# Optimization experiments

Hardware: AMD Instinct MI355X
Metric: run time of the kernel (lower is better)

The kernel has to match this reference:

```python
import jax, jax.numpy as jnp
import numpy as np

BS, SEQ, VOCAB, EMS, NHID, ML = 32, 512, 5000, 256, 512, 16
TEMP = 0.9
GAMMA = 0.0  # self.gamma is a fixed zero Variable in the original


def setup_inputs() -> dict:
    key = jax.random.key(0)
    ks = jax.random.split(key, 10)
    nm = SEQ // ML
    inputs = jax.random.randint(ks[0], (BS, SEQ), 0, VOCAB, dtype=jnp.int32)
    measure_steps = jax.random.randint(ks[1], (ML, BS, nm), 0, VOCAB, dtype=jnp.int32)
    measure_weights = jax.random.normal(ks[2], (BS, nm, nm), dtype=jnp.float32)
    h0 = jnp.zeros((BS, NHID), jnp.float32)
    c0 = jnp.zeros((BS, NHID), jnp.float32)
    initrange = 0.1
    emb = jax.random.uniform(ks[3], (VOCAB, EMS), minval=-initrange, maxval=initrange)
    k = 1.0 / np.sqrt(NHID).astype(np.float32)
    W_ih = jax.random.uniform(ks[4], (4 * NHID, EMS), minval=-k, maxval=k)
    W_hh = jax.random.uniform(ks[5], (4 * NHID, NHID), minval=-k, maxval=k)
    b_ih = jax.random.uniform(ks[6], (4 * NHID,), minval=-k, maxval=k)
    b_hh = jax.random.uniform(ks[7], (4 * NHID,), minval=-k, maxval=k)
    W_dec = jax.random.uniform(ks[8], (VOCAB, NHID), minval=-initrange, maxval=initrange)
    b_dec = jnp.zeros((VOCAB,), jnp.float32)
    return dict(inputs=inputs, h0=h0, c0=c0, measure_weights=measure_weights,
                measure_steps=measure_steps, emb=emb, W_ih=W_ih, W_hh=W_hh,
                b_ih=b_ih, b_hh=b_hh, W_dec=W_dec, b_dec=b_dec, measure_length=ML)


def _forward(h0, c0, mw, emb, W_ih, W_hh, b_ih, b_hh, W_dec, b_dec,
             inputs, msteps, measure_length):
    bs, seq = inputs.shape
    nm = seq // measure_length
    # attention over previous measures: softmax over j < m (causal-masked)
    mask = (jnp.arange(nm)[None, :] < jnp.arange(nm)[:, None]).astype(mw.dtype)  # [m, j]
    logits = jnp.where(mask[None] > 0, mw / TEMP, -1e9)
    sm = jax.nn.softmax(logits, axis=-1) * mask[None]  # [bs, m, j]
    prev_embs = emb[msteps]  # [ML, bs, nm, E]
    # lookback embedding for (measure m, step s): sum_j sm[b,m,j] * emb[steps[s,b,j]]
    lb = jnp.einsum('bmj,sbje->msbe', sm, prev_embs)  # [nm, ML, bs, E]
    lb_seq = lb.reshape(seq, bs, -1)  # time-major: t = m*ML + s
    # per-step bmm decode against embedding table: [bs, seq, V]
    lookback = jnp.einsum('tbe,ve->btv', lb_seq, emb)
    # original zeros lookback for timesteps with int(i/num_measures)==0, i.e. i < nm
    tmask = (jnp.arange(seq) >= nm)[None, :, None]
    lookback = jnp.where(tmask, lookback, jnp.zeros((), lookback.dtype))

    x = emb[inputs]  # [bs, seq, E] (single channel -> concat is identity)

    def cell(carry, xt):
        h, c = carry
        g = xt @ W_ih.T + b_ih + h @ W_hh.T + b_hh
        i, f, gg, o = jnp.split(g, 4, axis=-1)
        c2 = jax.nn.sigmoid(f) * c + jax.nn.sigmoid(i) * jnp.tanh(gg)
        h2 = jax.nn.sigmoid(o) * jnp.tanh(c2)
        return (h2, c2), h2

    (hT, cT), hs = jax.lax.scan(cell, (h0, c0), jnp.swapaxes(x, 0, 1))
    out = jnp.swapaxes(hs, 0, 1)  # [bs, seq, nhid]
    decoded = out @ W_dec.T + b_dec  # [bs, seq, V]
    dec = (1.0 - GAMMA) * decoded + GAMMA * lookback
    return dec, hT, cT


def reference(inputs, h0, c0, measure_weights, measure_steps, emb,
              W_ih, W_hh, b_ih, b_hh, W_dec, b_dec, measure_length):
    return _forward(h0, c0, measure_weights, emb, W_ih, W_hh, b_ih, b_hh,
                    W_dec, b_dec, inputs, measure_steps, measure_length)
```

## Files before the change

### kernel.cpp

```cpp
#include <hip/hip_runtime.h>
#include <cstdint>
#include <cstddef>

#define BS     32
#define SEQ    512
#define VOCAB  5000
#define EMS    256
#define NHID   512
#define GH     2048
#define NWG    32
#define SLICE  16
#define VPAD   5120
#define NBLK   256
#define NDEC   (NBLK - NWG)
#define NTILE  ((BS*SEQ/128) * (VPAD/128))

#define WS_FLAGS 0
#define WS_BIAS  2048
#define WS_WIH   (WS_BIAS + GH*4)
#define WS_WHH   (WS_WIH + GH*EMS*2)
#define WS_WDH   (WS_WHH + GH*NHID*2)
#define WS_WDL   (WS_WDH + VPAD*NHID*2)
#define WS_X     (WS_WDL + VPAD*NHID*2)
#define WS_HHI   (WS_X + SEQ*BS*EMS*2)
#define WS_HLO   (WS_HHI + BS*SEQ*NHID*2)
#define WS_HBUF  (WS_HLO + BS*SEQ*NHID*2)
#define WS_END   (WS_HBUF + 2*BS*NHID*2)

typedef float f32x4 __attribute__((ext_vector_type(4)));
typedef __bf16 bf16x8 __attribute__((ext_vector_type(8)));

static __device__ __forceinline__ uint16_t f2bf(float x) {
  uint32_t u = __builtin_bit_cast(uint32_t, x);
  u += 0x7FFFu + ((u >> 16) & 1u);
  return (uint16_t)(u >> 16);
}
static __device__ __forceinline__ float bf2f(uint16_t b) {
  return __builtin_bit_cast(float, (uint32_t)b << 16);
}
static __device__ __forceinline__ float sigf(float x) { return 1.0f / (1.0f + __expf(-x)); }
static __device__ __forceinline__ float tanhf_fast(float x) {
  return 1.0f - 2.0f / (__expf(2.0f * x) + 1.0f);
}
static __device__ __forceinline__ f32x4 mfma16(uint4 a, uint4 b, f32x4 c) {
  return __builtin_amdgcn_mfma_f32_16x16x32_bf16(
      __builtin_bit_cast(bf16x8, a), __builtin_bit_cast(bf16x8, b), c, 0, 0, 0);
}
static __device__ __forceinline__ void glds16(const void* g, void* l) {
  __builtin_amdgcn_global_load_lds((__attribute__((address_space(1))) void*)g,
                                   (__attribute__((address_space(3))) void*)l,
                                   16, 0, 0);
}
static __device__ __forceinline__ void coh_store_u32(uint32_t* p, uint32_t v) {
  __hip_atomic_store(p, v, __ATOMIC_RELAXED, __HIP_MEMORY_SCOPE_AGENT);
}

__global__ __launch_bounds__(256) void prep_kernel(
    const int* __restrict__ inputs, const float* __restrict__ h0,
    const float* __restrict__ emb, const float* __restrict__ Wih,
    const float* __restrict__ Whh, const float* __restrict__ bih,
    const float* __restrict__ bhh, const float* __restrict__ Wd,
    char* __restrict__ ws) {
  int gid = blockIdx.x * 256 + threadIdx.x;
  int gsz = gridDim.x * 256;
  uint16_t* wX  = (uint16_t*)(ws + WS_X);
  uint16_t* wIH = (uint16_t*)(ws + WS_WIH);
  uint16_t* wHH = (uint16_t*)(ws + WS_WHH);
  uint16_t* wDH = (uint16_t*)(ws + WS_WDH);
  uint16_t* wDL = (uint16_t*)(ws + WS_WDL);
  float*    bias = (float*)(ws + WS_BIAS);
  uint16_t* hb  = (uint16_t*)(ws + WS_HBUF);
  if (gid < 512) ((uint32_t*)(ws + WS_FLAGS))[gid] = 0u;
  for (int i = gid; i < SEQ*BS*EMS; i += gsz) {
    int e = i & (EMS-1), b = (i >> 8) & (BS-1), t = i >> 13;
    wX[i] = f2bf(emb[(size_t)inputs[b*SEQ + t] * EMS + e]);
  }
  for (int i = gid; i < GH*EMS; i += gsz)  wIH[i] = f2bf(Wih[i]);
  for (int i = gid; i < GH*NHID; i += gsz) wHH[i] = f2bf(Whh[i]);
  for (int i = gid; i < VPAD*NHID; i += gsz) {
    int row = i >> 9;
    uint16_t hi = 0, lo = 0;
    if (row < VOCAB) {
      float x = Wd[i];
      hi = f2bf(x);
      lo = f2bf(x - bf2f(hi));
    }
    wDH[i] = hi; wDL[i] = lo;
  }
  for (int i = gid; i < GH; i += gsz) bias[i] = bih[i] + bhh[i];
  for (int i = gid; i < BS*NHID; i += gsz) hb[i] = f2bf(h0[i]);
}

__global__ __launch_bounds__(256, 1) void fused_kernel(
    char* __restrict__ ws, const float* __restrict__ c0,
    const float* __restrict__ bdec, float* __restrict__ out,
    float* __restrict__ outT) {
  __shared__ __align__(16) char smem[104 * 1024];
  uint32_t* flags = (uint32_t*)(ws + WS_FLAGS);
  const int tid = threadIdx.x;
  const int lane = tid & 63, w = tid >> 6;

  if (blockIdx.x < NWG) {
    char* sW = smem;
    char* sH = smem + 64*1024;
    float* sG = (float*)(smem + 96*1024);
    const uint16_t* wHH = (const uint16_t*)(ws + WS_WHH);
    const uint16_t* wIH = (const uint16_t*)(ws + WS_WIH);
    const uint16_t* wX  = (const uint16_t*)(ws + WS_X);
    const float* bias = (const float*)(ws + WS_BIAS);
    uint16_t* hbuf = (uint16_t*)(ws + WS_HBUF);
    uint16_t* Hhi  = (uint16_t*)(ws + WS_HHI);
    uint16_t* Hlo  = (uint16_t*)(ws + WS_HLO);
    const int wg = blockIdx.x;
    const int mw = w >> 1, nw = w & 1;

    for (int c = tid; c < 4096; c += 256) {
      int row = c >> 6;
      int kb = (c & 63) * 16;
      int G = row >> 4, dl = row & 15;
      uint4 v = *(const uint4*)(wHH + (size_t)(G*NHID + wg*SLICE + dl) * NHID + kb/2);
      *(uint4*)(sW + row*1024 + (kb ^ ((row & 7) << 4))) = v;
    }
    const int bq = tid >> 3, dq = (tid & 7) * 2;
    float c_0 = c0[bq*NHID + wg*SLICE + dq];
    float c_1 = c0[bq*NHID + wg*SLICE + dq + 1];
    const int arow = mw*16 + (lane & 15);
    const int brow0 = (2*nw)*16 + (lane & 15);
    const int brow1 = brow0 + 16;
    const int kb0 = (lane >> 4) * 16;
    const int kfrag = (lane >> 4) * 8;
    const float bs0 = bias[(2*nw+0)*NHID + wg*SLICE + (lane & 15)];
    const float bs1 = bias[(2*nw+1)*NHID + wg*SLICE + (lane & 15)];
    uint4 wbf[2][8];
#pragma unroll
    for (int g = 0; g < 2; ++g)
#pragma unroll
      for (int k2 = 0; k2 < 8; ++k2)
        wbf[g][k2] = *(const uint4*)(wIH +
            (size_t)((2*nw+g)*NHID + wg*SLICE + (lane & 15)) * EMS + k2*32 + kfrag);
    uint4 xa[8], xb[8];
#pragma unroll
    for (int k2 = 0; k2 < 8; ++k2)
      xa[k2] = *(const uint4*)(wX + (size_t)arow * EMS + k2*32 + kfrag);
    __syncthreads();

    for (int t = 0; t < SEQ; ++t) {
      if (t > 0) {
        const uint32_t tgt = (uint32_t)t;
        const uint32_t* fp = flags + (lane & 31) * 16;
        uint32_t ptries = 0;
        for (;;) {
          uint32_t v = __hip_atomic_load(fp, __ATOMIC_RELAXED, __HIP_MEMORY_SCOPE_AGENT);
          if (__all((int)(v >= tgt))) break;
          if (++ptries > (1u << 20)) break;
        }
      }

      uint4 v0, v1, v2, v3, v4, v5, v6, v7;
      {
        const char* pb = (const char*)(hbuf + (t & 1) * (BS*NHID)) + tid * 16;
        asm volatile("global_load_dwordx4 %0, %1, off sc0 sc1" : "=v"(v0) : "v"(pb));
        asm volatile("global_load_dwordx4 %0, %1, off sc0 sc1" : "=v"(v1) : "v"(pb + 4096));
        asm volatile("global_load_dwordx4 %0, %1, off sc0 sc1" : "=v"(v2) : "v"(pb + 8192));
        asm volatile("global_load_dwordx4 %0, %1, off sc0 sc1" : "=v"(v3) : "v"(pb + 12288));
        asm volatile("global_load_dwordx4 %0, %1, off sc0 sc1" : "=v"(v4) : "v"(pb + 16384));
        asm volatile("global_load_dwordx4 %0, %1, off sc0 sc1" : "=v"(v5) : "v"(pb + 20480));
        asm volatile("global_load_dwordx4 %0, %1, off sc0 sc1" : "=v"(v6) : "v"(pb + 24576));
        asm volatile("global_load_dwordx4 %0, %1, off sc0 sc1" : "=v"(v7) : "v"(pb + 28672));
        const int tn = (t + 1 < SEQ) ? (t + 1) : 0;
        const uint16_t* xp = wX + (size_t)(tn*BS + arow) * EMS + kfrag;
        asm volatile("global_load_dwordx4 %0, %1, off"             : "=v"(xb[0]) : "v"(xp));
        asm volatile("global_load_dwordx4 %0, %1, off offset:64"   : "=v"(xb[1]) : "v"(xp));
        asm volatile("global_load_dwordx4 %0, %1, off offset:128"  : "=v"(xb[2]) : "v"(xp));
        asm volatile("global_load_dwordx4 %0, %1, off offset:192"  : "=v"(xb[3]) : "v"(xp));
        asm volatile("global_load_dwordx4 %0, %1, off offset:256"  : "=v"(xb[4]) : "v"(xp));
        asm volatile("global_load_dwordx4 %0, %1, off offset:320"  : "=v"(xb[5]) : "v"(xp));
        asm volatile("global_load_dwordx4 %0, %1, off offset:384"  : "=v"(xb[6]) : "v"(xp));
        asm volatile("global_load_dwordx4 %0, %1, off offset:448"  : "=v"(xb[7]) : "v"(xp));
      }
      f32x4 acc0, acc1;
#pragma unroll
      for (int r = 0; r < 4; ++r) { acc0[r] = bs0; acc1[r] = bs1; }
#pragma unroll
      for (int k2 = 0; k2 < 8; ++k2) {
        acc0 = mfma16(xa[k2], wbf[0][k2], acc0);
        acc1 = mfma16(xa[k2], wbf[1][k2], acc1);
      }
      asm volatile("s_waitcnt vmcnt(8)" ::: "memory");
      __builtin_amdgcn_sched_barrier(0);
      {
        const int kb = (tid & 63) * 16;
        const int ww = tid >> 6;
#define STW(J, VJ) *(uint4*)(sH + ((J)*4 + ww)*1024 + (kb ^ ((((J)&1)*4 + ww) << 4))) = VJ;
        STW(0, v0) STW(1, v1) STW(2, v2) STW(3, v3)
        STW(4, v4) STW(5, v5) STW(6, v6) STW(7, v7)
#undef STW
      }
      __syncthreads();

#pragma unroll
      for (int kt = 0; kt < 16; ++kt) {
        int kb = kt*64 + kb0;
        uint4 av = *(const uint4*)(sH + arow*1024 + (kb ^ ((arow & 7) << 4)));
        uint4 b0 = *(const uint4*)(sW + brow0*1024 + (kb ^ ((brow0 & 7) << 4)));
        uint4 b1 = *(const uint4*)(sW + brow1*1024 + (kb ^ ((brow1 & 7) << 4)));
        acc0 = mfma16(av, b0, acc0);
        acc1 = mfma16(av, b1, acc1);
      }
#pragma unroll
      for (int r = 0; r < 4; ++r) {
        int b = mw*16 + (lane >> 4)*4 + r;
        sG[((2*nw+0)*BS + b)*SLICE + (lane & 15)] = acc0[r];
        sG[((2*nw+1)*BS + b)*SLICE + (lane & 15)] = acc1[r];
      }
#pragma unroll
      for (int k2 = 0; k2 < 8; ++k2) xa[k2] = xb[k2];
      __syncthreads();

      float gi0 = sG[(0*BS + bq)*SLICE + dq], gi1 = sG[(0*BS + bq)*SLICE + dq + 1];
      float gf0 = sG[(1*BS + bq)*SLICE + dq], gf1 = sG[(1*BS + bq)*SLICE + dq + 1];
      float gg0 = sG[(2*BS + bq)*SLICE + dq], gg1 = sG[(2*BS + bq)*SLICE + dq + 1];
      float go0 = sG[(3*BS + bq)*SLICE + dq], go1 = sG[(3*BS + bq)*SLICE + dq + 1];
      c_0 = sigf(gf0)*c_0 + sigf(gi0)*tanhf_fast(gg0);
      c_1 = sigf(gf1)*c_1 + sigf(gi1)*tanhf_fast(gg1);
      float h_0 = sigf(go0)*tanhf_fast(c_0);
      float h_1 = sigf(go1)*tanhf_fast(c_1);

      uint16_t hh0 = f2bf(h_0), hh1 = f2bf(h_1);
      uint32_t hp = (uint32_t)hh0 | ((uint32_t)hh1 << 16);
      coh_store_u32((uint32_t*)(hbuf + ((t+1) & 1)*(BS*NHID)) +
                        ((bq*NHID + wg*SLICE + dq) >> 1), hp);
      size_t hoff = ((size_t)t*BS + bq)*NHID + wg*SLICE + dq;
      coh_store_u32((uint32_t*)(Hhi + hoff), hp);
      uint32_t lp = (uint32_t)f2bf(h_0 - bf2f(hh0)) | ((uint32_t)f2bf(h_1 - bf2f(hh1)) << 16);
      coh_store_u32((uint32_t*)(Hlo + hoff), lp);
      if (t == SEQ-1) {
        outT[bq*NHID + wg*SLICE + dq]     = h_0;
        outT[bq*NHID + wg*SLICE + dq + 1] = h_1;
        outT[BS*NHID + bq*NHID + wg*SLICE + dq]     = c_0;
        outT[BS*NHID + bq*NHID + wg*SLICE + dq + 1] = c_1;
      }

      __syncthreads();
      if (tid == 0)
        __hip_atomic_store(flags + wg * 16, (uint32_t)(t + 1),
                           __ATOMIC_RELAXED, __HIP_MEMORY_SCOPE_AGENT);
    }
  } else {
    char* lds = smem;
    const uint16_t* Hhi = (const uint16_t*)(ws + WS_HHI);
    const uint16_t* Hlo = (const uint16_t*)(ws + WS_HLO);
    const uint16_t* WDH = (const uint16_t*)(ws + WS_WDH);
    const uint16_t* WDL = (const uint16_t*)(ws + WS_WDL);
    const int widx = (int)blockIdx.x - NWG;
    const int wbase = (tid & ~63);
    const int mq = (w >> 1) * 64, nq = (w & 1) * 64;

    for (int q = widx; q < NTILE; q += NDEC) {
      const int mt = q / 40, nt = q % 40;
      const int m0 = mt * 128, n0 = nt * 128;
      if (w == 0) {
        const uint32_t tgt = (uint32_t)(mt*4 + 4);
        const uint32_t* fp = flags + (lane & 31) * 16;
        uint32_t tries = 0;
        for (;;) {
          uint32_t v = __hip_atomic_load(fp, __ATOMIC_RELAXED, __HIP_MEMORY_SCOPE_AGENT);
          if (__all((int)(v >= tgt))) break;
          __builtin_amdgcn_s_sleep(64);
          if (++tries > (1u << 14)) break;
        }
      }
      __syncthreads();

      auto stage = [&](int buf, int kk) {
        char* base = lds + buf * 32768;
#pragma unroll
        for (int c2 = 0; c2 < 2; ++c2) {
          int idx = c2*256 + tid;
          int row = idx >> 2, col = (idx & 3) * 8;
          int ldst = (c2*256 + wbase) * 16;
          glds16(Hhi + (size_t)(m0 + row) * NHID + kk*32 + col, base + ldst);
          glds16(Hlo + (size_t)(m0 + row) * NHID + kk*32 + col, base + 8192 + ldst);
          glds16(WDH + (size_t)(n0 + row) * NHID + kk*32 + col, base + 16384 + ldst);
          glds16(WDL + (size_t)(n0 + row) * NHID + kk*32 + col, base + 24576 + ldst);
        }
      };

      const f32x4 zero = {0.f, 0.f, 0.f, 0.f};
      f32x4 acc[4][4];
#pragma unroll
      for (int i = 0; i < 4; ++i)
#pragma unroll
        for (int j = 0; j < 4; ++j) acc[i][j] = zero;

      stage(0, 0);
      for (int s = 0; s < 16; ++s) {
        __syncthreads();
        if (s + 1 < 16) stage((s + 1) & 1, s + 1);
        const char* cb = lds + (s & 1) * 32768;
        uint4 ahi[4], alo[4], bhi[4], blo[4];
#pragma unroll
        for (int i = 0; i < 4; ++i) {
          int aoff = (mq + i*16 + (lane & 15))*64 + (lane >> 4)*16;
          int boff = (nq + i*16 + (lane & 15))*64 + (lane >> 4)*16;
          ahi[i] = *(const uint4*)(cb + aoff);
          alo[i] = *(const uint4*)(cb + 8192 + aoff);
          bhi[i] = *(const uint4*)(cb + 16384 + boff);
          blo[i] = *(const uint4*)(cb + 24576 + boff);
        }
#pragma unroll
        for (int i = 0; i < 4; ++i)
#pragma unroll
          for (int j = 0; j < 4; ++j) {
            acc[i][j] = mfma16(ahi[i], bhi[j], acc[i][j]);
            acc[i][j] = mfma16(ahi[i], blo[j], acc[i][j]);
            acc[i][j] = mfma16(alo[i], bhi[j], acc[i][j]);
          }
      }
#pragma unroll
      for (int j = 0; j < 4; ++j) {
        int V = n0 + nq + j*16 + (lane & 15);
        if (V >= VOCAB) continue;
        float bv = bdec[V];
#pragma unroll
        for (int i = 0; i < 4; ++i) {
          int Rb = m0 + mq + i*16 + (lane >> 4)*4;
#pragma unroll
          for (int r = 0; r < 4; ++r) {
            int rr = Rb + r;
            int orow = (rr & 31) * SEQ + (rr >> 5);
            out[(size_t)orow * VOCAB + V] = acc[i][j][r] + bv;
          }
        }
      }
      __syncthreads();
    }
  }
}

extern "C" void kernel_launch(void* const* d_in, const int* in_sizes, int n_in,
                              void* d_out, int out_size, void* d_ws, size_t ws_size,
                              hipStream_t stream) {
  (void)in_sizes; (void)n_in; (void)out_size; (void)ws_size;
  const int*   inputs = (const int*)  d_in[0];
  const float* h0     = (const float*)d_in[1];
  const float* c0     = (const float*)d_in[2];
  const float* emb    = (const float*)d_in[5];
  const float* Wih    = (const float*)d_in[6];
  const float* Whh    = (const float*)d_in[7];
  const float* bih    = (const float*)d_in[8];
  const float* bhh    = (const float*)d_in[9];
  const float* Wdec   = (const float*)d_in[10];
  const float* bdec   = (const float*)d_in[11];
  char* ws   = (char*)d_ws;
  float* out = (float*)d_out;
  float* outT = out + (size_t)BS*SEQ*VOCAB;

  prep_kernel<<<512, 256, 0, stream>>>(inputs, h0, emb, Wih, Whh, bih, bhh, Wdec, ws);
  fused_kernel<<<NBLK, 256, 0, stream>>>(ws, c0, bdec, out, outT);
}
```

Measured before the change: 2.085 ms.

## Split fused persistent kernel into separate LSTM scan and decoder GEMM kernels

Replaces the single persistent kernel, where 32 blocks ran the LSTM recurrence while the other blocks polled flags and decoded tiles as they became ready, with two launches: a 32-block scan kernel and a full-grid decode GEMM kernel. Hidden states are now stored batch-major with plain stores instead of coherent stores. This lets the decoder write output rows contiguously and use a swizzled tile order. The decode kernel now uses all CUs without flag waits, but decoding no longer overlaps with the serial recurrence, so the decoder GEMM time is added after the scan.

```diff
diff --git a/kernel.cpp b/kernel.cpp
--- a/kernel.cpp
+++ b/kernel.cpp
@@ -11,8 +11,6 @@
 #define NWG    32
 #define SLICE  16
 #define VPAD   5120
-#define NBLK   256
-#define NDEC   (NBLK - NWG)
 #define NTILE  ((BS*SEQ/128) * (VPAD/128))
 
 #define WS_FLAGS 0
@@ -91,249 +89,231 @@
   for (int i = gid; i < BS*NHID; i += gsz) hb[i] = f2bf(h0[i]);
 }
 
-__global__ __launch_bounds__(256, 1) void fused_kernel(
-    char* __restrict__ ws, const float* __restrict__ c0,
-    const float* __restrict__ bdec, float* __restrict__ out,
-    float* __restrict__ outT) {
-  __shared__ __align__(16) char smem[104 * 1024];
+__global__ __launch_bounds__(256, 1) void scan_kernel(
+    char* __restrict__ ws, const float* __restrict__ c0, float* __restrict__ outT) {
+  __shared__ __align__(16) char sW[64*1024];
+  __shared__ __align__(16) char sH[32*1024];
+  __shared__ float sG[4*BS*SLICE];
   uint32_t* flags = (uint32_t*)(ws + WS_FLAGS);
+  const uint16_t* wHH = (const uint16_t*)(ws + WS_WHH);
+  const uint16_t* wIH = (const uint16_t*)(ws + WS_WIH);
+  const uint16_t* wX  = (const uint16_t*)(ws + WS_X);
+  const float* bias = (const float*)(ws + WS_BIAS);
+  uint16_t* hbuf = (uint16_t*)(ws + WS_HBUF);
+  uint16_t* Hhi  = (uint16_t*)(ws + WS_HHI);
+  uint16_t* Hlo  = (uint16_t*)(ws + WS_HLO);
+  const int tid = threadIdx.x, wg = blockIdx.x;
+  const int lane = tid & 63, w = tid >> 6;
+  const int mw = w >> 1, nw = w & 1;
+
+  for (int c = tid; c < 4096; c += 256) {
+    int row = c >> 6;
+    int kb = (c & 63) * 16;
+    int G = row >> 4, dl = row & 15;
+    uint4 v = *(const uint4*)(wHH + (size_t)(G*NHID + wg*SLICE + dl) * NHID + kb/2);
+    *(uint4*)(sW + row*1024 + (kb ^ ((row & 7) << 4))) = v;
+  }
+  const int bq = tid >> 3, dq = (tid & 7) * 2;
+  float c_0 = c0[bq*NHID + wg*SLICE + dq];
+  float c_1 = c0[bq*NHID + wg*SLICE + dq + 1];
+  const int arow = mw*16 + (lane & 15);
+  const int brow0 = (2*nw)*16 + (lane & 15);
+  const int brow1 = brow0 + 16;
+  const int kb0 = (lane >> 4) * 16;
+  const int kfrag = (lane >> 4) * 8;
+  const float bs0 = bias[(2*nw+0)*NHID + wg*SLICE + (lane & 15)];
+  const float bs1 = bias[(2*nw+1)*NHID + wg*SLICE + (lane & 15)];
+  uint4 wbf[2][8];
+#pragma unroll
+  for (int g = 0; g < 2; ++g)
+#pragma unroll
+    for (int k2 = 0; k2 < 8; ++k2)
+      wbf[g][k2] = *(const uint4*)(wIH +
+          (size_t)((2*nw+g)*NHID + wg*SLICE + (lane & 15)) * EMS + k2*32 + kfrag);
+  uint4 xa[8], xb[8];
+#pragma unroll
+  for (int k2 = 0; k2 < 8; ++k2)
+    xa[k2] = *(const uint4*)(wX + (size_t)arow * EMS + k2*32 + kfrag);
+  __syncthreads();
+
+  for (int t = 0; t < SEQ; ++t) {
+    if (t > 0) {
+      const uint32_t tgt = (uint32_t)t;
+      const uint32_t* fp = flags + (lane & 31) * 16;
+      uint32_t ptries = 0;
+      for (;;) {
+        uint32_t v = __hip_atomic_load(fp, __ATOMIC_RELAXED, __HIP_MEMORY_SCOPE_AGENT);
+        if (__all((int)(v >= tgt))) break;
+        if (++ptries > (1u << 20)) break;
+      }
+    }
+
+    uint4 v0, v1, v2, v3, v4, v5, v6, v7;
+    {
+      const char* pb = (const char*)(hbuf + (t & 1) * (BS*NHID)) + tid * 16;
+      asm volatile("global_load_dwordx4 %0, %1, off sc0 sc1" : "=v"(v0) : "v"(pb));
+      asm volatile("global_load_dwordx4 %0, %1, off sc0 sc1" : "=v"(v1) : "v"(pb + 4096));
+      asm volatile("global_load_dwordx4 %0, %1, off sc0 sc1" : "=v"(v2) : "v"(pb + 8192));
+      asm volatile("global_load_dwordx4 %0, %1, off sc0 sc1" : "=v"(v3) : "v"(pb + 12288));
+      asm volatile("global_load_dwordx4 %0, %1, off sc0 sc1" : "=v"(v4) : "v"(pb + 16384));
+      asm volatile("global_load_dwordx4 %0, %1, off sc0 sc1" : "=v"(v5) : "v"(pb + 20480));
+      asm volatile("global_load_dwordx4 %0, %1, off sc0 sc1" : "=v"(v6) : "v"(pb + 24576));
+      asm volatile("global_load_dwordx4 %0, %1, off sc0 sc1" : "=v"(v7) : "v"(pb + 28672));
+      const int tn = (t + 1 < SEQ) ? (t + 1) : 0;
+      const uint16_t* xp = wX + (size_t)(tn*BS + arow) * EMS + kfrag;
+      asm volatile("global_load_dwordx4 %0, %1, off"             : "=v"(xb[0]) : "v"(xp));
+      asm volatile("global_load_dwordx4 %0, %1, off offset:64"   : "=v"(xb[1]) : "v"(xp));
+      asm volatile("global_load_dwordx4 %0, %1, off offset:128"  : "=v"(xb[2]) : "v"(xp));
+      asm volatile("global_load_dwordx4 %0, %1, off offset:192"  : "=v"(xb[3]) : "v"(xp));
+      asm volatile("global_load_dwordx4 %0, %1, off offset:256"  : "=v"(xb[4]) : "v"(xp));
+      asm volatile("global_load_dwordx4 %0, %1, off offset:320"  : "=v"(xb[5]) : "v"(xp));
+      asm volatile("global_load_dwordx4 %0, %1, off offset:384"  : "=v"(xb[6]) : "v"(xp));
+      asm volatile("global_load_dwordx4 %0, %1, off offset:448"  : "=v"(xb[7]) : "v"(xp));
+    }
+    f32x4 acc0, acc1;
+#pragma unroll
+    for (int r = 0; r < 4; ++r) { acc0[r] = bs0; acc1[r] = bs1; }
+#pragma unroll
+    for (int k2 = 0; k2 < 8; ++k2) {
+      acc0 = mfma16(xa[k2], wbf[0][k2], acc0);
+      acc1 = mfma16(xa[k2], wbf[1][k2], acc1);
+    }
+    asm volatile("s_waitcnt vmcnt(8)" ::: "memory");
+    __builtin_amdgcn_sched_barrier(0);
+    {
+      const int kb = (tid & 63) * 16;
+      const int ww = tid >> 6;
+#define STW(J, VJ) *(uint4*)(sH + ((J)*4 + ww)*1024 + (kb ^ ((((J)&1)*4 + ww) << 4))) = VJ;
+      STW(0, v0) STW(1, v1) STW(2, v2) STW(3, v3)
+      STW(4, v4) STW(5, v5) STW(6, v6) STW(7, v7)
+#undef STW
+    }
+    __syncthreads();
+
+#pragma unroll
+    for (int kt = 0; kt < 16; ++kt) {
+      int kb = kt*64 + kb0;
+      uint4 av = *(const uint4*)(sH + arow*1024 + (kb ^ ((arow & 7) << 4)));
+      uint4 b0 = *(const uint4*)(sW + brow0*1024 + (kb ^ ((brow0 & 7) << 4)));
+      uint4 b1 = *(const uint4*)(sW + brow1*1024 + (kb ^ ((brow1 & 7) << 4)));
+      acc0 = mfma16(av, b0, acc0);
+      acc1 = mfma16(av, b1, acc1);
+    }
+#pragma unroll
+    for (int r = 0; r < 4; ++r) {
+      int b = mw*16 + (lane >> 4)*4 + r;
+      sG[((2*nw+0)*BS + b)*SLICE + (lane & 15)] = acc0[r];
+      sG[((2*nw+1)*BS + b)*SLICE + (lane & 15)] = acc1[r];
+    }
+    asm volatile("s_waitcnt vmcnt(0)" ::: "memory");
+#pragma unroll
+    for (int k2 = 0; k2 < 8; ++k2) xa[k2] = xb[k2];
+    __syncthreads();
+
+    float gi0 = sG[(0*BS + bq)*SLICE + dq], gi1 = sG[(0*BS + bq)*SLICE + dq + 1];
+    float gf0 = sG[(1*BS + bq)*SLICE + dq], gf1 = sG[(1*BS + bq)*SLICE + dq + 1];
+    float gg0 = sG[(2*BS + bq)*SLICE + dq], gg1 = sG[(2*BS + bq)*SLICE + dq + 1];
+    float go0 = sG[(3*BS + bq)*SLICE + dq], go1 = sG[(3*BS + bq)*SLICE + dq + 1];
+    c_0 = sigf(gf0)*c_0 + sigf(gi0)*tanhf_fast(gg0);
+    c_1 = sigf(gf1)*c_1 + sigf(gi1)*tanhf_fast(gg1);
+    float h_0 = sigf(go0)*tanhf_fast(c_0);
+    float h_1 = sigf(go1)*tanhf_fast(c_1);
+
+    uint16_t hh0 = f2bf(h_0), hh1 = f2bf(h_1);
+    uint32_t hp = (uint32_t)hh0 | ((uint32_t)hh1 << 16);
+    coh_store_u32((uint32_t*)(hbuf + ((t+1) & 1)*(BS*NHID)) +
+                      ((bq*NHID + wg*SLICE + dq) >> 1), hp);
+    size_t hoff = ((size_t)bq*SEQ + t)*NHID + wg*SLICE + dq;
+    *(uint32_t*)(Hhi + hoff) = hp;
+    uint32_t lp = (uint32_t)f2bf(h_0 - bf2f(hh0)) | ((uint32_t)f2bf(h_1 - bf2f(hh1)) << 16);
+    *(uint32_t*)(Hlo + hoff) = lp;
+    if (t == SEQ-1) {
+      outT[bq*NHID + wg*SLICE + dq]     = h_0;
+      outT[bq*NHID + wg*SLICE + dq + 1] = h_1;
+      outT[BS*NHID + bq*NHID + wg*SLICE + dq]     = c_0;
+      outT[BS*NHID + bq*NHID + wg*SLICE + dq + 1] = c_1;
+    }
+
+    __syncthreads();
+    if (tid == 0)
+      __hip_atomic_store(flags + wg * 16, (uint32_t)(t + 1),
+                         __ATOMIC_RELAXED, __HIP_MEMORY_SCOPE_AGENT);
+  }
+}
+
+__global__ __launch_bounds__(256) void decode_kernel(
+    const char* __restrict__ ws, const float* __restrict__ bdec,
+    float* __restrict__ out) {
+  __shared__ __align__(16) char lds[2][32768];
+  const uint16_t* Hhi = (const uint16_t*)(ws + WS_HHI);
+  const uint16_t* Hlo = (const uint16_t*)(ws + WS_HLO);
+  const uint16_t* WDH = (const uint16_t*)(ws + WS_WDH);
+  const uint16_t* WDL = (const uint16_t*)(ws + WS_WDL);
   const int tid = threadIdx.x;
   const int lane = tid & 63, w = tid >> 6;
-
-  if (blockIdx.x < NWG) {
-    char* sW = smem;
-    char* sH = smem + 64*1024;
-    float* sG = (float*)(smem + 96*1024);
-    const uint16_t* wHH = (const uint16_t*)(ws + WS_WHH);
-    const uint16_t* wIH = (const uint16_t*)(ws + WS_WIH);
-    const uint16_t* wX  = (const uint16_t*)(ws + WS_X);
-    const float* bias = (const float*)(ws + WS_BIAS);
-    uint16_t* hbuf = (uint16_t*)(ws + WS_HBUF);
-    uint16_t* Hhi  = (uint16_t*)(ws + WS_HHI);
-    uint16_t* Hlo  = (uint16_t*)(ws + WS_HLO);
-    const int wg = blockIdx.x;
-    const int mw = w >> 1, nw = w & 1;
-
-    for (int c = tid; c < 4096; c += 256) {
-      int row = c >> 6;
-      int kb = (c & 63) * 16;
-      int G = row >> 4, dl = row & 15;
-      uint4 v = *(const uint4*)(wHH + (size_t)(G*NHID + wg*SLICE + dl) * NHID + kb/2);
-      *(uint4*)(sW + row*1024 + (kb ^ ((row & 7) << 4))) = v;
-    }
-    const int bq = tid >> 3, dq = (tid & 7) * 2;
-    float c_0 = c0[bq*NHID + wg*SLICE + dq];
-    float c_1 = c0[bq*NHID + wg*SLICE + dq + 1];
-    const int arow = mw*16 + (lane & 15);
-    const int brow0 = (2*nw)*16 + (lane & 15);
-    const int brow1 = brow0 + 16;
-    const int kb0 = (lane >> 4) * 16;
-    const int kfrag = (lane >> 4) * 8;
-    const float bs0 = bias[(2*nw+0)*NHID + wg*SLICE + (lane & 15)];
-    const float bs1 = bias[(2*nw+1)*NHID + wg*SLICE + (lane & 15)];
-    uint4 wbf[2][8];
-#pragma unroll
-    for (int g = 0; g < 2; ++g)
-#pragma unroll
-      for (int k2 = 0; k2 < 8; ++k2)
-        wbf[g][k2] = *(const uint4*)(wIH +
-            (size_t)((2*nw+g)*NHID + wg*SLICE + (lane & 15)) * EMS + k2*32 + kfrag);
-    uint4 xa[8], xb[8];
-#pragma unroll
-    for (int k2 = 0; k2 < 8; ++k2)
-      xa[k2] = *(const uint4*)(wX + (size_t)arow * EMS + k2*32 + kfrag);
+  const int wbase = (tid & ~63);
+  const int mq = (w >> 1) * 64, nq = (w & 1) * 64;
+  const int bid = (int)blockIdx.x;
+  const int swz = (bid & 7) * (NTILE / 8) + (bid >> 3);
+  const int mt = swz / 40, nt = swz % 40;
+  const int m0 = mt * 128, n0 = nt * 128;
+
+  auto stage = [&](int buf, int kk) {
+    char* base = &lds[buf][0];
+#pragma unroll
+    for (int c2 = 0; c2 < 2; ++c2) {
+      int idx = c2*256 + tid;
+      int row = idx >> 2, col = (idx & 3) * 8;
+      int ldst = (c2*256 + wbase) * 16;
+      glds16(Hhi + (size_t)(m0 + row) * NHID + kk*32 + col, base + ldst);
+      glds16(Hlo + (size_t)(m0 + row) * NHID + kk*32 + col, base + 8192 + ldst);
+      glds16(WDH + (size_t)(n0 + row) * NHID + kk*32 + col, base + 16384 + ldst);
+      glds16(WDL + (size_t)(n0 + row) * NHID + kk*32 + col, base + 24576 + ldst);
+    }
+  };
+
+  const f32x4 zero = {0.f, 0.f, 0.f, 0.f};
+  f32x4 acc[4][4];
+#pragma unroll
+  for (int i = 0; i < 4; ++i)
+#pragma unroll
+    for (int j = 0; j < 4; ++j) acc[i][j] = zero;
+
+  stage(0, 0);
+  for (int s = 0; s < 16; ++s) {
     __syncthreads();
-
-    for (int t = 0; t < SEQ; ++t) {
-      if (t > 0) {
-        const uint32_t tgt = (uint32_t)t;
-        const uint32_t* fp = flags + (lane & 31) * 16;
-        uint32_t ptries = 0;
-        for (;;) {
-          uint32_t v = __hip_atomic_load(fp, __ATOMIC_RELAXED, __HIP_MEMORY_SCOPE_AGENT);
-          if (__all((int)(v >= tgt))) break;
-          if (++ptries > (1u << 20)) break;
-        }
+    if (s + 1 < 16) stage((s + 1) & 1, s + 1);
+    const char* cb = &lds[s & 1][0];
+    uint4 ahi[4], alo[4], bhi[4], blo[4];
+#pragma unroll
+    for (int i = 0; i < 4; ++i) {
+      int aoff = (mq + i*16 + (lane & 15))*64 + (lane >> 4)*16;
+      int boff = (nq + i*16 + (lane & 15))*64 + (lane >> 4)*16;
+      ahi[i] = *(const uint4*)(cb + aoff);
+      alo[i] = *(const uint4*)(cb + 8192 + aoff);
+      bhi[i] = *(const uint4*)(cb + 16384 + boff);
+      blo[i] = *(const uint4*)(cb + 24576 + boff);
+    }
+#pragma unroll
+    for (int i = 0; i < 4; ++i)
+#pragma unroll
+      for (int j = 0; j < 4; ++j) {
+        acc[i][j] = mfma16(ahi[i], bhi[j], acc[i][j]);
+        acc[i][j] = mfma16(ahi[i], blo[j], acc[i][j]);
+        acc[i][j] = mfma16(alo[i], bhi[j], acc[i][j]);
       }
-
-      uint4 v0, v1, v2, v3, v4, v5, v6, v7;
-      {
-        const char* pb = (const char*)(hbuf + (t & 1) * (BS*NHID)) + tid * 16;
-        asm volatile("global_load_dwordx4 %0, %1, off sc0 sc1" : "=v"(v0) : "v"(pb));
-        asm volatile("global_load_dwordx4 %0, %1, off sc0 sc1" : "=v"(v1) : "v"(pb + 4096));
-        asm volatile("global_load_dwordx4 %0, %1, off sc0 sc1" : "=v"(v2) : "v"(pb + 8192));
-        asm volatile("global_load_dwordx4 %0, %1, off sc0 sc1" : "=v"(v3) : "v"(pb + 12288));
-        asm volatile("global_load_dwordx4 %0, %1, off sc0 sc1" : "=v"(v4) : "v"(pb + 16384));
-        asm volatile("global_load_dwordx4 %0, %1, off sc0 sc1" : "=v"(v5) : "v"(pb + 20480));
-        asm volatile("global_load_dwordx4 %0, %1, off sc0 sc1" : "=v"(v6) : "v"(pb + 24576));
-        asm volatile("global_load_dwordx4 %0, %1, off sc0 sc1" : "=v"(v7) : "v"(pb + 28672));
-        const int tn = (t + 1 < SEQ) ? (t + 1) : 0;
-        const uint16_t* xp = wX + (size_t)(tn*BS + arow) * EMS + kfrag;
-        asm volatile("global_load_dwordx4 %0, %1, off"             : "=v"(xb[0]) : "v"(xp));
-        asm volatile("global_load_dwordx4 %0, %1, off offset:64"   : "=v"(xb[1]) : "v"(xp));
-        asm volatile("global_load_dwordx4 %0, %1, off offset:128"  : "=v"(xb[2]) : "v"(xp));
-        asm volatile("global_load_dwordx4 %0, %1, off offset:192"  : "=v"(xb[3]) : "v"(xp));
-        asm volatile("global_load_dwordx4 %0, %1, off offset:256"  : "=v"(xb[4]) : "v"(xp));
-        asm volatile("global_load_dwordx4 %0, %1, off offset:320"  : "=v"(xb[5]) : "v"(xp));
-        asm volatile("global_load_dwordx4 %0, %1, off offset:384"  : "=v"(xb[6]) : "v"(xp));
-        asm volatile("global_load_dwordx4 %0, %1, off offset:448"  : "=v"(xb[7]) : "v"(xp));
-      }
-      f32x4 acc0, acc1;
-#pragma unroll
-      for (int r = 0; r < 4; ++r) { acc0[r] = bs0; acc1[r] = bs1; }
-#pragma unroll
-      for (int k2 = 0; k2 < 8; ++k2) {
-        acc0 = mfma16(xa[k2], wbf[0][k2], acc0);
-        acc1 = mfma16(xa[k2], wbf[1][k2], acc1);
-      }
-      asm volatile("s_waitcnt vmcnt(8)" ::: "memory");
-      __builtin_amdgcn_sched_barrier(0);
-      {
-        const int kb = (tid & 63) * 16;
-        const int ww = tid >> 6;
-#define STW(J, VJ) *(uint4*)(sH + ((J)*4 + ww)*1024 + (kb ^ ((((J)&1)*4 + ww) << 4))) = VJ;
-        STW(0, v0) STW(1, v1) STW(2, v2) STW(3, v3)
-        STW(4, v4) STW(5, v5) STW(6, v6) STW(7, v7)
-#undef STW
-      }
-      __syncthreads();
-
-#pragma unroll
-      for (int kt = 0; kt < 16; ++kt) {
-        int kb = kt*64 + kb0;
-        uint4 av = *(const uint4*)(sH + arow*1024 + (kb ^ ((arow & 7) << 4)));
-        uint4 b0 = *(const uint4*)(sW + brow0*1024 + (kb ^ ((brow0 & 7) << 4)));
-        uint4 b1 = *(const uint4*)(sW + brow1*1024 + (kb ^ ((brow1 & 7) << 4)));
-        acc0 = mfma16(av, b0, acc0);
-        acc1 = mfma16(av, b1, acc1);
-      }
-#pragma unroll
-      for (int r = 0; r < 4; ++r) {
-        int b = mw*16 + (lane >> 4)*4 + r;
-        sG[((2*nw+0)*BS + b)*SLICE + (lane & 15)] = acc0[r];
-        sG[((2*nw+1)*BS + b)*SLICE + (lane & 15)] = acc1[r];
-      }
-#pragma unroll
-      for (int k2 = 0; k2 < 8; ++k2) xa[k2] = xb[k2];
-      __syncthreads();
-
-      float gi0 = sG[(0*BS + bq)*SLICE + dq], gi1 = sG[(0*BS + bq)*SLICE + dq + 1];
-      float gf0 = sG[(1*BS + bq)*SLICE + dq], gf1 = sG[(1*BS + bq)*SLICE + dq + 1];
-      float gg0 = sG[(2*BS + bq)*SLICE + dq], gg1 = sG[(2*BS + bq)*SLICE + dq + 1];
-      float go0 = sG[(3*BS + bq)*SLICE + dq], go1 = sG[(3*BS + bq)*SLICE + dq + 1];
-      c_0 = sigf(gf0)*c_0 + sigf(gi0)*tanhf_fast(gg0);
-      c_1 = sigf(gf1)*c_1 + sigf(gi1)*tanhf_fast(gg1);
-      float h_0 = sigf(go0)*tanhf_fast(c_0);
-      float h_1 = sigf(go1)*tanhf_fast(c_1);
-
-      uint16_t hh0 = f2bf(h_0), hh1 = f2bf(h_1);
-      uint32_t hp = (uint32_t)hh0 | ((uint32_t)hh1 << 16);
-      coh_store_u32((uint32_t*)(hbuf + ((t+1) & 1)*(BS*NHID)) +
-                        ((bq*NHID + wg*SLICE + dq) >> 1), hp);
-      size_t hoff = ((size_t)t*BS + bq)*NHID + wg*SLICE + dq;
-      coh_store_u32((uint32_t*)(Hhi + hoff), hp);
-      uint32_t lp = (uint32_t)f2bf(h_0 - bf2f(hh0)) | ((uint32_t)f2bf(h_1 - bf2f(hh1)) << 16);
-      coh_store_u32((uint32_t*)(Hlo + hoff), lp);
-      if (t == SEQ-1) {
-        outT[bq*NHID + wg*SLICE + dq]     = h_0;
-        outT[bq*NHID + wg*SLICE + dq + 1] = h_1;
-        outT[BS*NHID + bq*NHID + wg*SLICE + dq]     = c_0;
-        outT[BS*NHID + bq*NHID + wg*SLICE + dq + 1] = c_1;
-      }
-
-      __syncthreads();
-      if (tid == 0)
-        __hip_atomic_store(flags + wg * 16, (uint32_t)(t + 1),
-                           __ATOMIC_RELAXED, __HIP_MEMORY_SCOPE_AGENT);
-    }
-  } else {
-    char* lds = smem;
-    const uint16_t* Hhi = (const uint16_t*)(ws + WS_HHI);
-    const uint16_t* Hlo = (const uint16_t*)(ws + WS_HLO);
-    const uint16_t* WDH = (const uint16_t*)(ws + WS_WDH);
-    const uint16_t* WDL = (const uint16_t*)(ws + WS_WDL);
-    const int widx = (int)blockIdx.x - NWG;
-    const int wbase = (tid & ~63);
-    const int mq = (w >> 1) * 64, nq = (w & 1) * 64;
-
-    for (int q = widx; q < NTILE; q += NDEC) {
-      const int mt = q / 40, nt = q % 40;
-      const int m0 = mt * 128, n0 = nt * 128;
-      if (w == 0) {
-        const uint32_t tgt = (uint32_t)(mt*4 + 4);
-        const uint32_t* fp = flags + (lane & 31) * 16;
-        uint32_t tries = 0;
-        for (;;) {
-          uint32_t v = __hip_atomic_load(fp, __ATOMIC_RELAXED, __HIP_MEMORY_SCOPE_AGENT);
-          if (__all((int)(v >= tgt))) break;
-          __builtin_amdgcn_s_sleep(64);
-          if (++tries > (1u << 14)) break;
-        }
-      }
-      __syncthreads();
-
-      auto stage = [&](int buf, int kk) {
-        char* base = lds + buf * 32768;
-#pragma unroll
-        for (int c2 = 0; c2 < 2; ++c2) {
-          int idx = c2*256 + tid;
-          int row = idx >> 2, col = (idx & 3) * 8;
-          int ldst = (c2*256 + wbase) * 16;
-          glds16(Hhi + (size_t)(m0 + row) * NHID + kk*32 + col, base + ldst);
-          glds16(Hlo + (size_t)(m0 + row) * NHID + kk*32 + col, base + 8192 + ldst);
-          glds16(WDH + (size_t)(n0 + row) * NHID + kk*32 + col, base + 16384 + ldst);
-          glds16(WDL + (size_t)(n0 + row) * NHID + kk*32 + col, base + 24576 + ldst);
-        }
-      };
-
-      const f32x4 zero = {0.f, 0.f, 0.f, 0.f};
-      f32x4 acc[4][4];
-#pragma unroll
-      for (int i = 0; i < 4; ++i)
-#pragma unroll
-        for (int j = 0; j < 4; ++j) acc[i][j] = zero;
-
-      stage(0, 0);
-      for (int s = 0; s < 16; ++s) {
-        __syncthreads();
-        if (s + 1 < 16) stage((s + 1) & 1, s + 1);
-        const char* cb = lds + (s & 1) * 32768;
-        uint4 ahi[4], alo[4], bhi[4], blo[4];
-#pragma unroll
-        for (int i = 0; i < 4; ++i) {
-          int aoff = (mq + i*16 + (lane & 15))*64 + (lane >> 4)*16;
-          int boff = (nq + i*16 + (lane & 15))*64 + (lane >> 4)*16;
-          ahi[i] = *(const uint4*)(cb + aoff);
-          alo[i] = *(const uint4*)(cb + 8192 + aoff);
-          bhi[i] = *(const uint4*)(cb + 16384 + boff);
-          blo[i] = *(const uint4*)(cb + 24576 + boff);
-        }
-#pragma unroll
-        for (int i = 0; i < 4; ++i)
-#pragma unroll
-          for (int j = 0; j < 4; ++j) {
-            acc[i][j] = mfma16(ahi[i], bhi[j], acc[i][j]);
-            acc[i][j] = mfma16(ahi[i], blo[j], acc[i][j]);
-            acc[i][j] = mfma16(alo[i], bhi[j], acc[i][j]);
-          }
-      }
-#pragma unroll
-      for (int j = 0; j < 4; ++j) {
-        int V = n0 + nq + j*16 + (lane & 15);
-        if (V >= VOCAB) continue;
-        float bv = bdec[V];
-#pragma unroll
-        for (int i = 0; i < 4; ++i) {
-          int Rb = m0 + mq + i*16 + (lane >> 4)*4;
-#pragma unroll
-          for (int r = 0; r < 4; ++r) {
-            int rr = Rb + r;
-            int orow = (rr & 31) * SEQ + (rr >> 5);
-            out[(size_t)orow * VOCAB + V] = acc[i][j][r] + bv;
-          }
-        }
-      }
-      __syncthreads();
+  }
+#pragma unroll
+  for (int j = 0; j < 4; ++j) {
+    int V = n0 + nq + j*16 + (lane & 15);
+    if (V >= VOCAB) continue;
+    float bv = bdec[V];
+#pragma unroll
+    for (int i = 0; i < 4; ++i) {
+      int Rb = m0 + mq + i*16 + (lane >> 4)*4;
+#pragma unroll
+      for (int r = 0; r < 4; ++r)
+        out[(size_t)(Rb + r) * VOCAB + V] = acc[i][j][r] + bv;
     }
   }
 }
@@ -357,5 +337,6 @@
   float* outT = out + (size_t)BS*SEQ*VOCAB;
 
   prep_kernel<<<512, 256, 0, stream>>>(inputs, h0, emb, Wih, Whh, bih, bhh, Wdec, ws);
-  fused_kernel<<<NBLK, 256, 0, stream>>>(ws, c0, bdec, out, outT);
-}
+  scan_kernel<<<NWG, 256, 0, stream>>>(ws, c0, outT);
+  decode_kernel<<<NTILE, 256, 0, stream>>>(ws, bdec, out);
+}
```

Result: slower. 2.339 ms (+12.2%).
